# Kernel tuning notes

Measured on AMD Instinct MI355X. Metric: run time of the kernel, lower is better.

The kernel has to match this reference:

```python
import jax, jax.numpy as jnp
import numpy as np

DILATION = 1
THETA = 1.0
K = 3 + 2 * (DILATION - 1)  # 3x3 window


def setup_inputs() -> dict:
    key = jax.random.key(0)
    x = jax.random.normal(key, (8, 64, 224, 224), dtype=jnp.float32)
    return {"x": x}


def _extract_patches(x, k, d):
    # x: [b, c, h, w] -> patches: [b, c, k*k, h, w], zero-padded like F.unfold(padding=d)
    b, c, h, w = x.shape
    xp = jnp.pad(x, ((0, 0), (0, 0), (d, d), (d, d)))
    return jnp.stack(
        [xp[:, :, i * d:i * d + h, j * d:j * d + w] for i in range(k) for j in range(k)],
        axis=2,
    )


def reference(x) -> jnp.ndarray:
    b, c, h, w = x.shape
    patches = _extract_patches(x, K, DILATION)  # [b, c, kk, h, w]

    mean = patches.mean(axis=2, keepdims=True)
    # torch .std() is unbiased (ddof=1)
    std = jnp.clip(jnp.std(patches, axis=2, keepdims=True, ddof=1), 1e-3, None)
    normed = (patches - mean) / std

    contrast = (normed ** 2).mean(axis=2)
    energy = (patches ** 2).mean(axis=2)
    clamped = jnp.clip(patches, 1e-6, None)
    entropy = -(clamped * jnp.log(clamped)).mean(axis=2)
    homogeneity = 1.0 / ((1.0 + jnp.abs(patches - mean)).mean(axis=2) + 1e-6)

    feats = jnp.stack([contrast, energy, entropy, homogeneity], axis=2)  # [b, c, 4, h, w]

    log_feat = jnp.log(jnp.clip(feats, 1e-5, None))
    martingale = jnp.clip(jnp.exp(THETA * log_feat - 0.5 * THETA ** 2), 1e-4, 1e4)
    martingale = jnp.where(jnp.isfinite(martingale), martingale, jnp.ones_like(martingale))

    # per-channel feature stacks concatenated along channel dim -> [b, c*4, h, w]
    return martingale.reshape(b, c * 4, h, w)
```

## Files before the change

### kernel.cpp

```cpp
#include <hip/hip_runtime.h>
#include <math.h>

#define B 8
#define C 64
#define H 224
#define W 224
#define HW (H * W)
#define TW 32
#define TH 32
#define HS 4

__global__ __launch_bounds__(64, 4) void medseg_kernel(const float* __restrict__ x,
                                                       float* __restrict__ out) {
    const int plane = blockIdx.z;
    const int w0 = blockIdx.x * TW;
    const int tid = threadIdx.x;
    const int tx = tid & 7;
    const int g  = tid >> 3;
    const int cb = w0 + 4 * tx;
    const int h0 = blockIdx.y * TH + g * HS;

    const float* __restrict__ xp = x + (size_t)plane * HW;
    const float4 Z = make_float4(0.f, 0.f, 0.f, 0.f);

    const bool lb = (cb > 0);
    const bool rb = (cb + 4 < W);

    float win[3][12];
    float re[3][6];

    auto loadrow = [&](int r, float w[12]) {
        const bool rin = (r >= 0) && (r < H);
        const float* rowp = xp + r * W;
        float4 a = (rin && lb) ? *(const float4*)(rowp + cb - 4) : Z;
        float4 b = rin         ? *(const float4*)(rowp + cb)     : Z;
        float4 c = (rin && rb) ? *(const float4*)(rowp + cb + 4) : Z;
        w[0] = a.x; w[1] = a.y; w[2]  = a.z; w[3]  = a.w;
        w[4] = b.x; w[5] = b.y; w[6]  = b.z; w[7]  = b.w;
        w[8] = c.x; w[9] = c.y; w[10] = c.z; w[11] = c.w;
    };
    auto rowstats = [&](const float w[12], float e[6]) {
        #pragma unroll
        for (int j = 0; j < 6; ++j) {
            const float c0 = fmaxf(w[j + 3], 1e-6f);
            e[j] = c0 * __log2f(c0);
        }
    };

    loadrow(h0 - 1, win[0]);
    loadrow(h0,     win[1]);
    loadrow(h0 + 1, win[2]);
    rowstats(win[0], re[0]);
    rowstats(win[1], re[1]);
    rowstats(win[2], re[2]);

    const float EXPM  = 0.6065306597126334f;
    const float E9    = EXPM / 9.0f;
    const float NL9   = -0.6931471805599453f * EXPM / 9.0f;
    const float CONTR = 0.5391383641890075f;

    float* ob0 = out + ((size_t)plane * 4) * HW + (size_t)h0 * W + cb;

    #pragma unroll
    for (int it = 0; it < HS; ++it) {
        const int s0 = it % 3, s1 = (it + 1) % 3, s2 = (it + 2) % 3;

        float4 na = Z, nb = Z, nc = Z;
        if (it < HS - 1) {
            const int r = h0 + it + 2;
            const bool rin = (r < H);
            const float* rowp = xp + r * W;
            na = (rin && lb) ? *(const float4*)(rowp + cb - 4) : Z;
            nb = rin         ? *(const float4*)(rowp + cb)     : Z;
            nc = (rin && rb) ? *(const float4*)(rowp + cb + 4) : Z;
        }

        float cs[6], cq[6], ce[6];
        #pragma unroll
        for (int j = 0; j < 6; ++j) {
            const float v0 = win[s0][j + 3], v1 = win[s1][j + 3], v2 = win[s2][j + 3];
            cs[j] = v0 + v1 + v2;
            cq[j] = fmaf(v0, v0, fmaf(v1, v1, v2 * v2));
            ce[j] = re[s0][j] + (re[s1][j] + re[s2][j]);
        }

        float oe[4], ot[4], oh[4];
        #pragma unroll
        for (int k = 0; k < 4; ++k) {
            const float s1v = cs[k] + cs[k + 1] + cs[k + 2];
            const float s2v = cq[k] + cq[k + 1] + cq[k + 2];
            const float sev = ce[k] + ce[k + 1] + ce[k + 2];
            const float mean = s1v * (1.0f / 9.0f);

            float sad = 0.0f;
            #pragma unroll
            for (int j = 0; j < 3; ++j) sad += fabsf(win[s0][k + j + 3] - mean);
            #pragma unroll
            for (int j = 0; j < 3; ++j) sad += fabsf(win[s1][k + j + 3] - mean);
            #pragma unroll
            for (int j = 0; j < 3; ++j) sad += fabsf(win[s2][k + j + 3] - mean);

            oe[k] = fmaxf(s2v * E9, 1e-4f);
            ot[k] = fmaxf(sev * NL9, 1e-4f);
            const float denom = fmaf(sad, 1.0f / 9.0f, 1.000001f);
            oh[k] = fmaxf(EXPM * __builtin_amdgcn_rcpf(denom), 1e-4f);
        }

        float* ob = ob0 + (size_t)it * W;
        *(float4*)(ob + 0 * HW) = make_float4(CONTR, CONTR, CONTR, CONTR);
        *(float4*)(ob + 1 * HW) = make_float4(oe[0], oe[1], oe[2], oe[3]);
        *(float4*)(ob + 2 * HW) = make_float4(ot[0], ot[1], ot[2], ot[3]);
        *(float4*)(ob + 3 * HW) = make_float4(oh[0], oh[1], oh[2], oh[3]);

        if (it < HS - 1) {
            float* w = win[s0];
            w[0] = na.x; w[1] = na.y; w[2]  = na.z; w[3]  = na.w;
            w[4] = nb.x; w[5] = nb.y; w[6]  = nb.z; w[7]  = nb.w;
            w[8] = nc.x; w[9] = nc.y; w[10] = nc.z; w[11] = nc.w;
            rowstats(w, re[s0]);
        }
    }
}

extern "C" void kernel_launch(void* const* d_in, const int* in_sizes, int n_in,
                              void* d_out, int out_size, void* d_ws, size_t ws_size,
                              hipStream_t stream) {
    const float* x = (const float*)d_in[0];
    float* out = (float*)d_out;
    dim3 grid(W / TW, H / TH, B * C);
    dim3 block(64);
    medseg_kernel<<<grid, block, 0, stream>>>(x, out);
}
```

Measured before the change: 503.8 us.

## Use narrower halo loads, recompute entropy terms, and double threads per block

Each thread now keeps a 6-wide window per row, loading the centre float4 plus two scalar halo values instead of three float4s, which cuts load traffic and register use. The cached per-row entropy terms are dropped and the x*log(x) values are recomputed inside the column sums, trading extra log work for fewer live registers. Rows per thread go from 4 to 2 and the block grows to 128 threads with a higher occupancy hint, so the 32x32 tile is still covered with more parallelism. The cost is more redundant halo-row loads per output row and repeated log evaluations.

```diff
diff --git a/kernel.cpp b/kernel.cpp
--- a/kernel.cpp
+++ b/kernel.cpp
@@ -8,10 +8,12 @@
 #define HW (H * W)
 #define TW 32
 #define TH 32
-#define HS 4
+#define HS 2
 
-__global__ __launch_bounds__(64, 4) void medseg_kernel(const float* __restrict__ x,
-                                                       float* __restrict__ out) {
+typedef float v4f __attribute__((ext_vector_type(4)));
+
+__global__ __launch_bounds__(128, 8) void medseg_kernel(const float* __restrict__ x,
+                                                        float* __restrict__ out) {
     const int plane = blockIdx.z;
     const int w0 = blockIdx.x * TW;
     const int tid = threadIdx.x;
@@ -21,38 +23,23 @@
     const int h0 = blockIdx.y * TH + g * HS;
 
     const float* __restrict__ xp = x + (size_t)plane * HW;
-    const float4 Z = make_float4(0.f, 0.f, 0.f, 0.f);
-
     const bool lb = (cb > 0);
     const bool rb = (cb + 4 < W);
 
-    float win[3][12];
-    float re[3][6];
+    float win[3][6];
 
-    auto loadrow = [&](int r, float w[12]) {
+    auto loadrow = [&](int r, float w[6]) {
         const bool rin = (r >= 0) && (r < H);
         const float* rowp = xp + r * W;
-        float4 a = (rin && lb) ? *(const float4*)(rowp + cb - 4) : Z;
-        float4 b = rin         ? *(const float4*)(rowp + cb)     : Z;
-        float4 c = (rin && rb) ? *(const float4*)(rowp + cb + 4) : Z;
-        w[0] = a.x; w[1] = a.y; w[2]  = a.z; w[3]  = a.w;
-        w[4] = b.x; w[5] = b.y; w[6]  = b.z; w[7]  = b.w;
-        w[8] = c.x; w[9] = c.y; w[10] = c.z; w[11] = c.w;
-    };
-    auto rowstats = [&](const float w[12], float e[6]) {
-        #pragma unroll
-        for (int j = 0; j < 6; ++j) {
-            const float c0 = fmaxf(w[j + 3], 1e-6f);
-            e[j] = c0 * __log2f(c0);
-        }
+        float4 bq = rin ? *(const float4*)(rowp + cb) : make_float4(0.f, 0.f, 0.f, 0.f);
+        float al = (rin && lb) ? rowp[cb - 1] : 0.0f;
+        float cr = (rin && rb) ? rowp[cb + 4] : 0.0f;
+        w[0] = al; w[1] = bq.x; w[2] = bq.y; w[3] = bq.z; w[4] = bq.w; w[5] = cr;
     };
 
     loadrow(h0 - 1, win[0]);
     loadrow(h0,     win[1]);
     loadrow(h0 + 1, win[2]);
-    rowstats(win[0], re[0]);
-    rowstats(win[1], re[1]);
-    rowstats(win[2], re[2]);
 
     const float EXPM  = 0.6065306597126334f;
     const float E9    = EXPM / 9.0f;
@@ -65,23 +52,17 @@
     for (int it = 0; it < HS; ++it) {
         const int s0 = it % 3, s1 = (it + 1) % 3, s2 = (it + 2) % 3;
 
-        float4 na = Z, nb = Z, nc = Z;
-        if (it < HS - 1) {
-            const int r = h0 + it + 2;
-            const bool rin = (r < H);
-            const float* rowp = xp + r * W;
-            na = (rin && lb) ? *(const float4*)(rowp + cb - 4) : Z;
-            nb = rin         ? *(const float4*)(rowp + cb)     : Z;
-            nc = (rin && rb) ? *(const float4*)(rowp + cb + 4) : Z;
-        }
+        float pre[6];
+        if (it < HS - 1) loadrow(h0 + it + 2, pre);
 
         float cs[6], cq[6], ce[6];
         #pragma unroll
         for (int j = 0; j < 6; ++j) {
-            const float v0 = win[s0][j + 3], v1 = win[s1][j + 3], v2 = win[s2][j + 3];
+            const float v0 = win[s0][j], v1 = win[s1][j], v2 = win[s2][j];
             cs[j] = v0 + v1 + v2;
             cq[j] = fmaf(v0, v0, fmaf(v1, v1, v2 * v2));
-            ce[j] = re[s0][j] + (re[s1][j] + re[s2][j]);
+            const float c0 = fmaxf(v0, 1e-6f), c1 = fmaxf(v1, 1e-6f), c2 = fmaxf(v2, 1e-6f);
+            ce[j] = fmaf(c0, __log2f(c0), fmaf(c1, __log2f(c1), c2 * __log2f(c2)));
         }
 
         float oe[4], ot[4], oh[4];
@@ -94,11 +75,11 @@
 
             float sad = 0.0f;
             #pragma unroll
-            for (int j = 0; j < 3; ++j) sad += fabsf(win[s0][k + j + 3] - mean);
+            for (int j = 0; j < 3; ++j) sad += fabsf(win[s0][k + j] - mean);
             #pragma unroll
-            for (int j = 0; j < 3; ++j) sad += fabsf(win[s1][k + j + 3] - mean);
+            for (int j = 0; j < 3; ++j) sad += fabsf(win[s1][k + j] - mean);
             #pragma unroll
-            for (int j = 0; j < 3; ++j) sad += fabsf(win[s2][k + j + 3] - mean);
+            for (int j = 0; j < 3; ++j) sad += fabsf(win[s2][k + j] - mean);
 
             oe[k] = fmaxf(s2v * E9, 1e-4f);
             ot[k] = fmaxf(sev * NL9, 1e-4f);
@@ -107,17 +88,18 @@
         }
 
         float* ob = ob0 + (size_t)it * W;
-        *(float4*)(ob + 0 * HW) = make_float4(CONTR, CONTR, CONTR, CONTR);
-        *(float4*)(ob + 1 * HW) = make_float4(oe[0], oe[1], oe[2], oe[3]);
-        *(float4*)(ob + 2 * HW) = make_float4(ot[0], ot[1], ot[2], ot[3]);
-        *(float4*)(ob + 3 * HW) = make_float4(oh[0], oh[1], oh[2], oh[3]);
+        v4f vc = {CONTR, CONTR, CONTR, CONTR};
+        v4f ve = {oe[0], oe[1], oe[2], oe[3]};
+        v4f vt = {ot[0], ot[1], ot[2], ot[3]};
+        v4f vh = {oh[0], oh[1], oh[2], oh[3]};
+        *(v4f*)(ob + 0 * HW) = vc;
+        *(v4f*)(ob + 1 * HW) = ve;
+        *(v4f*)(ob + 2 * HW) = vt;
+        *(v4f*)(ob + 3 * HW) = vh;
 
         if (it < HS - 1) {
-            float* w = win[s0];
-            w[0] = na.x; w[1] = na.y; w[2]  = na.z; w[3]  = na.w;
-            w[4] = nb.x; w[5] = nb.y; w[6]  = nb.z; w[7]  = nb.w;
-            w[8] = nc.x; w[9] = nc.y; w[10] = nc.z; w[11] = nc.w;
-            rowstats(w, re[s0]);
+            #pragma unroll
+            for (int j = 0; j < 6; ++j) win[s0][j] = pre[j];
         }
     }
 }
@@ -128,6 +110,6 @@
     const float* x = (const float*)d_in[0];
     float* out = (float*)d_out;
     dim3 grid(W / TW, H / TH, B * C);
-    dim3 block(64);
+    dim3 block(128);
     medseg_kernel<<<grid, block, 0, stream>>>(x, out);
 }
```

After: 531.3 us. 5.4% more time.
